# Optimization experiments

Hardware: AMD Instinct MI355X
Metric: run time of the kernel (lower is better)

The kernel has to match this reference:

```python
import jax, jax.numpy as jnp
import numpy as np

BATCH = 4096
N_CLASSES = 512
INPUT_DIM = 256


def setup_inputs() -> dict:
    key = jax.random.key(0)
    kx, kw = jax.random.split(key)
    x = jax.random.normal(kx, (BATCH, INPUT_DIM), dtype=jnp.float32)
    W = 0.1 * jax.random.normal(kw, (N_CLASSES, INPUT_DIM), dtype=jnp.float32)
    b = jnp.zeros((N_CLASSES,), dtype=jnp.float32)
    return {"x": x, "W": W, "b": b}


def reference(x, W, b):
    # L1 distance between each row of x [B, D] and each class prototype W [C, D]
    # d: [B, C]; score is negative distance plus bias.
    d = jnp.sum(jnp.abs(W[None, :, :] - x[:, None, :]), axis=-1)
    return -d + b
```

## Files before the change

### kernel.cpp

```cpp
#include <hip/hip_runtime.h>


#define B_SZ 4096
#define C_SZ 512
#define D_SZ 256

constexpr int BM = 64;
constexpr int BN = 64;
constexpr int DK = 32;
constexpr int NP = DK / 2;
constexpr int NCHUNK = D_SZ / DK;

__device__ __forceinline__ unsigned int sad16(unsigned int a, unsigned int b, unsigned int c) {
#if __has_builtin(__builtin_amdgcn_sad_u16)
    return __builtin_amdgcn_sad_u16(a, b, c);
#else
    unsigned int d;
    asm("v_sad_u16 %0, %1, %2, %3" : "=v"(d) : "v"(a), "v"(b), "v"(c));
    return d;
#endif
}

__device__ __forceinline__ unsigned int q16(float v) {
    return (unsigned int)(v * 4096.0f + 32768.5f);
}
__device__ __forceinline__ unsigned int qpk(float a, float b) {
    return q16(a) | (q16(b) << 16);
}

__global__ __launch_bounds__(256)
void l1dist_sad_kernel(const float* __restrict__ x,
                       const float* __restrict__ W,
                       const float* __restrict__ bias,
                       float* __restrict__ out) {
    __shared__ __align__(16) unsigned int xs[2][NP][BM];
    __shared__ __align__(16) unsigned int ws[2][NP][BN];

    const int tid  = threadIdx.x;
    const int tx   = tid & 15;
    const int ty   = tid >> 4;
    const int brow = blockIdx.y * BM;
    const int bcol = blockIdx.x * BN;

    const int r = tid & 63;
    const int g = tid >> 6;

    const float* xrow = x + (brow + r) * D_SZ + g * 8;
    const float* wrow = W + (bcol + r) * D_SZ + g * 8;

    unsigned int acc[4][4];
    #pragma unroll
    for (int i = 0; i < 4; ++i)
        #pragma unroll
        for (int j = 0; j < 4; ++j) acc[i][j] = 0u;

    {
        float4 a0 = *reinterpret_cast<const float4*>(xrow + 0);
        float4 a1 = *reinterpret_cast<const float4*>(xrow + 4);
        float4 b0 = *reinterpret_cast<const float4*>(wrow + 0);
        float4 b1 = *reinterpret_cast<const float4*>(wrow + 4);
        xs[0][g * 4 + 0][r] = qpk(a0.x, a0.y);
        xs[0][g * 4 + 1][r] = qpk(a0.z, a0.w);
        xs[0][g * 4 + 2][r] = qpk(a1.x, a1.y);
        xs[0][g * 4 + 3][r] = qpk(a1.z, a1.w);
        ws[0][g * 4 + 0][r] = qpk(b0.x, b0.y);
        ws[0][g * 4 + 1][r] = qpk(b0.z, b0.w);
        ws[0][g * 4 + 2][r] = qpk(b1.x, b1.y);
        ws[0][g * 4 + 3][r] = qpk(b1.z, b1.w);
    }

    for (int ck = 0; ck < NCHUNK; ++ck) {
        const int cur = ck & 1;

        float4 a0, a1, b0, b1;
        if (ck + 1 < NCHUNK) {
            const float* xn = xrow + (ck + 1) * DK;
            const float* wn = wrow + (ck + 1) * DK;
            a0 = *reinterpret_cast<const float4*>(xn + 0);
            a1 = *reinterpret_cast<const float4*>(xn + 4);
            b0 = *reinterpret_cast<const float4*>(wn + 0);
            b1 = *reinterpret_cast<const float4*>(wn + 4);
        }

        __syncthreads();

        #pragma unroll
        for (int dp = 0; dp < NP; ++dp) {
            uint4 xf = *reinterpret_cast<const uint4*>(&xs[cur][dp][ty * 4]);
            uint4 wf = *reinterpret_cast<const uint4*>(&ws[cur][dp][tx * 4]);
            unsigned int xa[4] = {xf.x, xf.y, xf.z, xf.w};
            unsigned int wa[4] = {wf.x, wf.y, wf.z, wf.w};
            #pragma unroll
            for (int i = 0; i < 4; ++i)
                #pragma unroll
                for (int j = 0; j < 4; ++j)
                    acc[i][j] = sad16(xa[i], wa[j], acc[i][j]);
        }

        if (ck + 1 < NCHUNK) {
            const int nb = cur ^ 1;
            xs[nb][g * 4 + 0][r] = qpk(a0.x, a0.y);
            xs[nb][g * 4 + 1][r] = qpk(a0.z, a0.w);
            xs[nb][g * 4 + 2][r] = qpk(a1.x, a1.y);
            xs[nb][g * 4 + 3][r] = qpk(a1.z, a1.w);
            ws[nb][g * 4 + 0][r] = qpk(b0.x, b0.y);
            ws[nb][g * 4 + 1][r] = qpk(b0.z, b0.w);
            ws[nb][g * 4 + 2][r] = qpk(b1.x, b1.y);
            ws[nb][g * 4 + 3][r] = qpk(b1.z, b1.w);
        }
    }

    const int col0 = bcol + tx * 4;
    float4 bv = *reinterpret_cast<const float4*>(&bias[col0]);
    float ba[4] = {bv.x, bv.y, bv.z, bv.w};
    constexpr float inv_scale = 1.0f / 4096.0f;
    #pragma unroll
    for (int i = 0; i < 4; ++i) {
        float4 o;
        o.x = ba[0] - (float)acc[i][0] * inv_scale;
        o.y = ba[1] - (float)acc[i][1] * inv_scale;
        o.z = ba[2] - (float)acc[i][2] * inv_scale;
        o.w = ba[3] - (float)acc[i][3] * inv_scale;
        *reinterpret_cast<float4*>(&out[(brow + ty * 4 + i) * C_SZ + col0]) = o;
    }
}

extern "C" void kernel_launch(void* const* d_in, const int* in_sizes, int n_in,
                              void* d_out, int out_size, void* d_ws, size_t ws_size,
                              hipStream_t stream) {
    const float* x    = (const float*)d_in[0];
    const float* W    = (const float*)d_in[1];
    const float* bias = (const float*)d_in[2];
    float* out        = (float*)d_out;

    dim3 grid(C_SZ / BN, B_SZ / BM);
    dim3 block(256);
    l1dist_sad_kernel<<<grid, block, 0, stream>>>(x, W, bias, out);
}
```

Before: 19.47 us.

## Split reduction dimension across wave halves with 512-thread blocks and shuffle reduce

Doubles the block to 512 threads and gives each half-wave half of the packed-dimension pairs in every chunk, so each thread issues half as many SAD ops per chunk. Partial sums are combined with a cross-lane xor-32 shuffle, and each half-wave writes two of the four output rows. Per-thread global loads drop to one float4 per matrix per chunk. This adds parallelism and latency hiding per tile, at the cost of a shuffle reduction, more threads per block and possibly lower block residency.

Result: slower. 20.95 us (+7.6%).

```diff
diff --git a/kernel.cpp b/kernel.cpp
--- a/kernel.cpp
+++ b/kernel.cpp
@@ -28,25 +28,29 @@
     return q16(a) | (q16(b) << 16);
 }
 
-__global__ __launch_bounds__(256)
-void l1dist_sad_kernel(const float* __restrict__ x,
-                       const float* __restrict__ W,
-                       const float* __restrict__ bias,
-                       float* __restrict__ out) {
+__global__ __launch_bounds__(512)
+void l1dist_sad_ds2_kernel(const float* __restrict__ x,
+                           const float* __restrict__ W,
+                           const float* __restrict__ bias,
+                           float* __restrict__ out) {
     __shared__ __align__(16) unsigned int xs[2][NP][BM];
     __shared__ __align__(16) unsigned int ws[2][NP][BN];
 
     const int tid  = threadIdx.x;
-    const int tx   = tid & 15;
-    const int ty   = tid >> 4;
+    const int lane = tid & 63;
+    const int wv   = tid >> 6;
+    const int dg   = lane >> 5;
+    const int slot = wv * 32 + (lane & 31);
+    const int tx   = slot & 15;
+    const int ty   = slot >> 4;
     const int brow = blockIdx.y * BM;
     const int bcol = blockIdx.x * BN;
 
     const int r = tid & 63;
-    const int g = tid >> 6;
+    const int h = tid >> 6;
 
-    const float* xrow = x + (brow + r) * D_SZ + g * 8;
-    const float* wrow = W + (bcol + r) * D_SZ + g * 8;
+    const float* xrow = x + (brow + r) * D_SZ + h * 4;
+    const float* wrow = W + (bcol + r) * D_SZ + h * 4;
 
     unsigned int acc[4][4];
     #pragma unroll
@@ -55,37 +59,30 @@
         for (int j = 0; j < 4; ++j) acc[i][j] = 0u;
 
     {
-        float4 a0 = *reinterpret_cast<const float4*>(xrow + 0);
-        float4 a1 = *reinterpret_cast<const float4*>(xrow + 4);
-        float4 b0 = *reinterpret_cast<const float4*>(wrow + 0);
-        float4 b1 = *reinterpret_cast<const float4*>(wrow + 4);
-        xs[0][g * 4 + 0][r] = qpk(a0.x, a0.y);
-        xs[0][g * 4 + 1][r] = qpk(a0.z, a0.w);
-        xs[0][g * 4 + 2][r] = qpk(a1.x, a1.y);
-        xs[0][g * 4 + 3][r] = qpk(a1.z, a1.w);
-        ws[0][g * 4 + 0][r] = qpk(b0.x, b0.y);
-        ws[0][g * 4 + 1][r] = qpk(b0.z, b0.w);
-        ws[0][g * 4 + 2][r] = qpk(b1.x, b1.y);
-        ws[0][g * 4 + 3][r] = qpk(b1.z, b1.w);
+        float4 a = *reinterpret_cast<const float4*>(xrow);
+        float4 b = *reinterpret_cast<const float4*>(wrow);
+        xs[0][2 * h + 0][r] = qpk(a.x, a.y);
+        xs[0][2 * h + 1][r] = qpk(a.z, a.w);
+        ws[0][2 * h + 0][r] = qpk(b.x, b.y);
+        ws[0][2 * h + 1][r] = qpk(b.z, b.w);
     }
+
+    const int dpbase = dg * (NP / 2);
 
     for (int ck = 0; ck < NCHUNK; ++ck) {
         const int cur = ck & 1;
 
-        float4 a0, a1, b0, b1;
+        float4 a, b;
         if (ck + 1 < NCHUNK) {
-            const float* xn = xrow + (ck + 1) * DK;
-            const float* wn = wrow + (ck + 1) * DK;
-            a0 = *reinterpret_cast<const float4*>(xn + 0);
-            a1 = *reinterpret_cast<const float4*>(xn + 4);
-            b0 = *reinterpret_cast<const float4*>(wn + 0);
-            b1 = *reinterpret_cast<const float4*>(wn + 4);
+            a = *reinterpret_cast<const float4*>(xrow + (ck + 1) * DK);
+            b = *reinterpret_cast<const float4*>(wrow + (ck + 1) * DK);
         }
 
         __syncthreads();
 
         #pragma unroll
-        for (int dp = 0; dp < NP; ++dp) {
+        for (int p = 0; p < NP / 2; ++p) {
+            const int dp = dpbase + p;
             uint4 xf = *reinterpret_cast<const uint4*>(&xs[cur][dp][ty * 4]);
             uint4 wf = *reinterpret_cast<const uint4*>(&ws[cur][dp][tx * 4]);
             unsigned int xa[4] = {xf.x, xf.y, xf.z, xf.w};
@@ -99,23 +96,26 @@
 
         if (ck + 1 < NCHUNK) {
             const int nb = cur ^ 1;
-            xs[nb][g * 4 + 0][r] = qpk(a0.x, a0.y);
-            xs[nb][g * 4 + 1][r] = qpk(a0.z, a0.w);
-            xs[nb][g * 4 + 2][r] = qpk(a1.x, a1.y);
-            xs[nb][g * 4 + 3][r] = qpk(a1.z, a1.w);
-            ws[nb][g * 4 + 0][r] = qpk(b0.x, b0.y);
-            ws[nb][g * 4 + 1][r] = qpk(b0.z, b0.w);
-            ws[nb][g * 4 + 2][r] = qpk(b1.x, b1.y);
-            ws[nb][g * 4 + 3][r] = qpk(b1.z, b1.w);
+            xs[nb][2 * h + 0][r] = qpk(a.x, a.y);
+            xs[nb][2 * h + 1][r] = qpk(a.z, a.w);
+            ws[nb][2 * h + 0][r] = qpk(b.x, b.y);
+            ws[nb][2 * h + 1][r] = qpk(b.z, b.w);
         }
     }
+
+    #pragma unroll
+    for (int i = 0; i < 4; ++i)
+        #pragma unroll
+        for (int j = 0; j < 4; ++j)
+            acc[i][j] += (unsigned int)__shfl_xor((int)acc[i][j], 32, 64);
 
     const int col0 = bcol + tx * 4;
     float4 bv = *reinterpret_cast<const float4*>(&bias[col0]);
     float ba[4] = {bv.x, bv.y, bv.z, bv.w};
     constexpr float inv_scale = 1.0f / 4096.0f;
     #pragma unroll
-    for (int i = 0; i < 4; ++i) {
+    for (int k = 0; k < 2; ++k) {
+        const int i = dg * 2 + k;
         float4 o;
         o.x = ba[0] - (float)acc[i][0] * inv_scale;
         o.y = ba[1] - (float)acc[i][1] * inv_scale;
@@ -134,6 +134,6 @@
     float* out        = (float*)d_out;
 
     dim3 grid(C_SZ / BN, B_SZ / BM);
-    dim3 block(256);
-    l1dist_sad_kernel<<<grid, block, 0, stream>>>(x, W, bias, out);
+    dim3 block(512);
+    l1dist_sad_ds2_kernel<<<grid, block, 0, stream>>>(x, W, bias, out);
 }
```
